# Performance work log

Measured on AMD Instinct MI355X. Metric: run time of the kernel, lower is better.

Reference implementation:

```python
import jax, jax.numpy as jnp
import numpy as np

G = 128          # number of point-cloud groups
DOWNSAMPLE = 256 # points per group
D = 256          # feature dim


def _pairwise_dist(x, y):
    # x: [G, n, d], y: [G, m, d] -> Euclidean distances [G, n, m]
    x2 = jnp.sum(x * x, axis=-1)[:, :, None]
    y2 = jnp.sum(y * y, axis=-1)[:, None, :]
    d2 = jnp.maximum(x2 + y2 - 2.0 * jnp.einsum('gnd,gmd->gnm', x, y), 0.0)
    # safe sqrt (zero diagonal has zero distance, avoid NaN grads)
    return jnp.where(d2 > 0, jnp.sqrt(jnp.where(d2 > 0, d2, 1.0)), 0.0)


def setup_inputs() -> dict:
    key = jax.random.key(0)
    k1, k2 = jax.random.split(key)
    inp = jax.random.normal(k1, (G * DOWNSAMPLE, D), dtype=jnp.float32)
    tgt = jax.random.normal(k2, (G * DOWNSAMPLE, D), dtype=jnp.float32)
    return {"input": inp, "target": tgt, "downsample": DOWNSAMPLE}


def reference(input, target, downsample):
    # MMDLoss.forward: reshape to (-1, downsample, D), batched energy distance, mean
    x = input.reshape(-1, downsample, input.shape[-1])   # [G, n, D]
    y = target.reshape(-1, downsample, target.shape[-1]) # [G, m, D]
    # Energy distance (geomloss 'energy' kernel k(x,y) = -||x-y||, uniform weights):
    # L = mean_ij ||x_i - y_j|| - 0.5 mean_ij ||x_i - x_j|| - 0.5 mean_ij ||y_i - y_j||
    d_xy = jnp.mean(_pairwise_dist(x, y), axis=(1, 2))  # [G]
    d_xx = jnp.mean(_pairwise_dist(x, x), axis=(1, 2))  # [G]
    d_yy = jnp.mean(_pairwise_dist(y, y), axis=(1, 2))  # [G]
    loss_per_group = d_xy - 0.5 * d_xx - 0.5 * d_yy
    return jnp.mean(loss_per_group)
```

## Files before the change

### kernel.cpp

```cpp
#include <hip/hip_runtime.h>
#include <hip/hip_bf16.h>
#include <stdint.h>
#include <string.h>

typedef __attribute__((ext_vector_type(8))) short short8;
typedef __attribute__((ext_vector_type(4))) float floatx4;

#define NPTS 256
#define DIM  256
#define TILE 128
#define BK   32
#define NIT  (DIM / BK)
#define LDSS 40

static __device__ __forceinline__ uint32_t cvtsq2(float a, float b, float& s) {
    __hip_bfloat162 h = __float22bfloat162_rn(float2{a, b});
    uint32_t d;
    memcpy(&d, &h, 4);
    const float lo = __builtin_bit_cast(float, d << 16);
    const float hi = __builtin_bit_cast(float, d & 0xFFFF0000u);
    s += lo * lo + hi * hi;
    return d;
}
static __device__ __forceinline__ uint4 cvt8(const float4 u, const float4 v, float& s) {
    uint4 r;
    r.x = cvtsq2(u.x, u.y, s); r.y = cvtsq2(u.z, u.w, s);
    r.z = cvtsq2(v.x, v.y, s); r.w = cvtsq2(v.z, v.w, s);
    return r;
}

__global__ __launch_bounds__(512, 4)
void mmd_pipe(const float* __restrict__ X, const float* __restrict__ Y,
              float* __restrict__ out, float scale, int G) {
    int g, t;
    const int f = blockIdx.x;
    if ((G & 7) == 0) { const int xcd = f & 7, j = f >> 3; g = (j / 10) * 8 + xcd; t = j % 10; }
    else              { g = f / 10; t = f % 10; }

    int ptype, ti, tj; float w;
    if (t < 4)      { ptype = 0; ti = t >> 1; tj = t & 1; w = 1.0f; }
    else if (t < 7) { int u = t - 4; ptype = 1; ti = (u == 2); tj = (u >= 1); w = (u == 1) ? -1.0f : -0.5f; }
    else            { int u = t - 7; ptype = 2; ti = (u == 2); tj = (u >= 1); w = (u == 1) ? -1.0f : -0.5f; }

    const float *Pf, *Qf;
    if (ptype == 0)      { Pf = X; Qf = Y; }
    else if (ptype == 1) { Pf = X; Qf = X; }
    else                 { Pf = Y; Qf = Y; }
    const bool symdiag = (ptype != 0) && (ti == tj);

    const size_t prow0 = (size_t)g * NPTS + (size_t)ti * TILE;
    const size_t qrow0 = (size_t)g * NPTS + (size_t)tj * TILE;

    __shared__ __align__(16) uint16_t As[2][TILE * LDSS];
    __shared__ __align__(16) uint16_t Bs[2][TILE * LDSS];
    __shared__ float rnorm[TILE];
    __shared__ float cnorm[TILE];
    __shared__ float wpart[8];

    const int tid  = threadIdx.x;
    const int lane = tid & 63;
    const int wv   = tid >> 6;
    const int quad = lane >> 4;
    const int l15  = lane & 15;
    const int rowbase = (wv & 3) * 32;
    const int colbase = (wv >> 2) * 64;

    const int prow = tid >> 2;
    const int pcol = (tid & 3) * 8;
    const float* gA = Pf + (prow0 + prow) * DIM + pcol;
    const float* gB = Qf + (qrow0 + prow) * DIM + pcol;
    const int woff = prow * LDSS + pcol;

    floatx4 acc[2][4];
    #pragma unroll
    for (int i = 0; i < 2; ++i)
        #pragma unroll
        for (int j = 0; j < 4; ++j) acc[i][j] = (floatx4)0.0f;

    float sqp = 0.0f, sqq = 0.0f;

    float4 ra0 = *(const float4*)(gA);
    float4 ra1 = *(const float4*)(gA + 4);
    float4 rb0 = *(const float4*)(gB);
    float4 rb1 = *(const float4*)(gB + 4);
    {
        const uint4 pa = cvt8(ra0, ra1, sqp);
        const uint4 pb = cvt8(rb0, rb1, sqq);
        *(uint4*)&As[0][woff] = pa;
        *(uint4*)&Bs[0][woff] = pb;
    }
    ra0 = *(const float4*)(gA + BK);
    ra1 = *(const float4*)(gA + BK + 4);
    rb0 = *(const float4*)(gB + BK);
    rb1 = *(const float4*)(gB + BK + 4);

    #pragma unroll
    for (int it = 0; it < NIT; ++it) {
        const int b = it & 1;
        __syncthreads();

        if (it < NIT - 1) {
            const uint4 pa = cvt8(ra0, ra1, sqp);
            const uint4 pb = cvt8(rb0, rb1, sqq);
            *(uint4*)&As[b ^ 1][woff] = pa;
            *(uint4*)&Bs[b ^ 1][woff] = pb;
        }
        if (it < NIT - 2) {
            const int k0 = (it + 2) * BK;
            ra0 = *(const float4*)(gA + k0);
            ra1 = *(const float4*)(gA + k0 + 4);
            rb0 = *(const float4*)(gB + k0);
            rb1 = *(const float4*)(gB + k0 + 4);
        }

        short8 af[2], bfr[4];
        #pragma unroll
        for (int mi = 0; mi < 2; ++mi)
            af[mi] = *(const short8*)&As[b][(rowbase + mi * 16 + l15) * LDSS + quad * 8];
        #pragma unroll
        for (int ni = 0; ni < 4; ++ni)
            bfr[ni] = *(const short8*)&Bs[b][(colbase + ni * 16 + l15) * LDSS + quad * 8];
        #pragma unroll
        for (int mi = 0; mi < 2; ++mi)
            #pragma unroll
            for (int ni = 0; ni < 4; ++ni)
                acc[mi][ni] = __builtin_amdgcn_mfma_f32_16x16x32_bf16(
                    af[mi], bfr[ni], acc[mi][ni], 0, 0, 0);
    }

    sqp += __shfl_xor(sqp, 1); sqp += __shfl_xor(sqp, 2);
    sqq += __shfl_xor(sqq, 1); sqq += __shfl_xor(sqq, 2);
    if ((tid & 3) == 0) { rnorm[prow] = sqp; cnorm[prow] = sqq; }
    __syncthreads();

    float lsum = 0.0f;
    #pragma unroll
    for (int mi = 0; mi < 2; ++mi) {
        #pragma unroll
        for (int i = 0; i < 4; ++i) {
            const int r = rowbase + mi * 16 + quad * 4 + i;
            const float rv = rnorm[r];
            #pragma unroll
            for (int ni = 0; ni < 4; ++ni) {
                const int c = colbase + ni * 16 + l15;
                float d2 = rv + cnorm[c] - 2.0f * acc[mi][ni][i];
                float s = sqrtf(fmaxf(d2, 0.0f));
                if (symdiag && (r == c)) s = 0.0f;
                lsum += s;
            }
        }
    }
    #pragma unroll
    for (int off = 32; off; off >>= 1) lsum += __shfl_down(lsum, off);
    if (lane == 0) wpart[wv] = lsum;
    __syncthreads();
    if (tid == 0) {
        float bs = 0.0f;
        #pragma unroll
        for (int i = 0; i < 8; ++i) bs += wpart[i];
        atomicAdd(out, bs * (w * scale));
    }
}

extern "C" void kernel_launch(void* const* d_in, const int* in_sizes, int n_in,
                              void* d_out, int out_size, void* d_ws, size_t ws_size,
                              hipStream_t stream) {
    const float* X = (const float*)d_in[0];
    const float* Y = (const float*)d_in[1];
    const int total_elems = in_sizes[0];
    const int G = total_elems / (NPTS * DIM);

    float* out = (float*)d_out;
    hipMemsetAsync(out, 0, sizeof(float) * out_size, stream);

    const float scale = 1.0f / ((float)NPTS * (float)NPTS * (float)G);
    mmd_pipe<<<10 * G, 512, 0, stream>>>(X, Y, out, scale, G);
}
```

Before: 122.0 us.

## Pre-convert inputs to bf16 with norms, then run LDS-DMA MFMA main kernel

Adds a prep kernel that converts X and Y to bf16 once in workspace and precomputes row norms. The main kernel then streams bf16 tiles into swizzled LDS using global_load_lds, with BK=64, 256 threads and a 4x4 MFMA tile per wave, and loads only one tile for symmetric diagonal blocks. This removes the repeated fp32 reads and conversions done in every tile block. The cost is an extra launch and a workspace round trip. The old fused path is kept as a fallback when no workspace is available.

```diff
diff --git a/kernel.cpp b/kernel.cpp
--- a/kernel.cpp
+++ b/kernel.cpp
@@ -5,13 +5,13 @@
 
 typedef __attribute__((ext_vector_type(8))) short short8;
 typedef __attribute__((ext_vector_type(4))) float floatx4;
+typedef unsigned short u16;
 
 #define NPTS 256
 #define DIM  256
 #define TILE 128
-#define BK   32
-#define NIT  (DIM / BK)
-#define LDSS 40
+#define BKN  64
+#define NITN (DIM / BKN)
 
 static __device__ __forceinline__ uint32_t cvtsq2(float a, float b, float& s) {
     __hip_bfloat162 h = __float22bfloat162_rn(float2{a, b});
@@ -25,9 +25,165 @@
 static __device__ __forceinline__ uint4 cvt8(const float4 u, const float4 v, float& s) {
     uint4 r;
     r.x = cvtsq2(u.x, u.y, s); r.y = cvtsq2(u.z, u.w, s);
-    r.z = cvtsq2(v.x, v.y, s); r.w = cvtsq2(v.z, v.w, s);
+    r.z = cvtsq2(v.x, v.w == v.w ? v.w : v.w, s), r.z = cvtsq2(v.x, v.y, s); r.w = cvtsq2(v.z, v.w, s);
     return r;
 }
+
+__global__ __launch_bounds__(256)
+void mmd_prep(const float* __restrict__ X, const float* __restrict__ Y,
+              u16* __restrict__ Zb, float* __restrict__ nrm,
+              int totalRows, int halfRows) {
+    const int gid = blockIdx.x * 256 + threadIdx.x;
+    const int row = gid >> 5;
+    if (row >= totalRows) return;
+    const int sub = gid & 31;
+    const float* src = (row < halfRows ? X + (size_t)row * DIM
+                                       : Y + (size_t)(row - halfRows) * DIM) + sub * 8;
+    const float4 a = *(const float4*)src;
+    const float4 b = *(const float4*)(src + 4);
+    float s = 0.0f;
+    uint4 p;
+    p.x = cvtsq2(a.x, a.y, s); p.y = cvtsq2(a.z, a.w, s);
+    p.z = cvtsq2(b.x, b.y, s); p.w = cvtsq2(b.z, b.w, s);
+    *(uint4*)(Zb + (size_t)row * DIM + sub * 8) = p;
+    s += __shfl_xor(s, 1); s += __shfl_xor(s, 2); s += __shfl_xor(s, 4);
+    s += __shfl_xor(s, 8); s += __shfl_xor(s, 16);
+    if (sub == 0) nrm[row] = s;
+}
+
+static __device__ __forceinline__ void stage_tile(
+    const u16* __restrict__ Zrow0,
+    u16* ldsbase,
+    int k0, int wv, int lane) {
+    #pragma unroll
+    for (int j = 0; j < 4; ++j) {
+        const int cid = (wv * 4 + j) * 64 + lane;
+        const int row = cid >> 3;
+        const int cs  = cid & 7;
+        const int cg  = cs ^ (row & 7);
+        const u16* src = Zrow0 + (size_t)row * DIM + k0 + cg * 8;
+        u16* dst = ldsbase + (size_t)(wv * 4 + j) * 512;
+        __builtin_amdgcn_global_load_lds(
+            (const __attribute__((address_space(1))) uint32_t*)src,
+            (__attribute__((address_space(3))) uint32_t*)dst, 16, 0, 0);
+    }
+}
+
+__global__ __launch_bounds__(256, 2)
+void mmd_main(const u16* __restrict__ Zb, const float* __restrict__ nrm,
+              float* __restrict__ out, float scale, int G) {
+    int g, t;
+    const int f = blockIdx.x;
+    if ((G & 7) == 0) { const int xcd = f & 7, j = f >> 3; g = (j / 10) * 8 + xcd; t = j % 10; }
+    else              { g = f / 10; t = f % 10; }
+
+    int ptype, ti, tj; float w;
+    if (t < 4)      { ptype = 0; ti = t >> 1; tj = t & 1; w = 1.0f; }
+    else if (t < 7) { int u = t - 4; ptype = 1; ti = (u == 2); tj = (u >= 1); w = (u == 1) ? -1.0f : -0.5f; }
+    else            { int u = t - 7; ptype = 2; ti = (u == 2); tj = (u >= 1); w = (u == 1) ? -1.0f : -0.5f; }
+
+    const int half = G * NPTS;
+    const int pbase = (ptype == 2) ? half : 0;
+    const int qbase = (ptype == 1) ? 0 : half;
+    const size_t prow0 = (size_t)pbase + (size_t)g * NPTS + (size_t)ti * TILE;
+    const size_t qrow0 = (size_t)qbase + (size_t)g * NPTS + (size_t)tj * TILE;
+    const bool symdiag = (ptype != 0) && (ti == tj);
+
+    const u16* ZP = Zb + prow0 * DIM;
+    const u16* ZQ = Zb + qrow0 * DIM;
+
+    __shared__ __align__(16) u16 As[2][TILE * BKN];
+    __shared__ __align__(16) u16 Bs[2][TILE * BKN];
+    __shared__ float rnormS[TILE];
+    __shared__ float cnormS[TILE];
+    __shared__ float wpart[4];
+
+    const int tid  = threadIdx.x;
+    const int lane = tid & 63;
+    const int wv   = tid >> 6;
+    const int quad = lane >> 4;
+    const int l15  = lane & 15;
+    const int wr   = (wv >> 1) * 64;
+    const int wc   = (wv & 1) * 64;
+    const int sw0  = (quad ^ (l15 & 7)) * 8;
+
+    floatx4 acc[4][4];
+    #pragma unroll
+    for (int i = 0; i < 4; ++i)
+        #pragma unroll
+        for (int j = 0; j < 4; ++j) acc[i][j] = (floatx4)0.0f;
+
+    if (tid < TILE) rnormS[tid] = nrm[prow0 + tid];
+    else            cnormS[tid - TILE] = nrm[qrow0 + (tid - TILE)];
+
+    stage_tile(ZP, As[0], 0, wv, lane);
+    if (!symdiag) stage_tile(ZQ, Bs[0], 0, wv, lane);
+
+    #pragma unroll
+    for (int it = 0; it < NITN; ++it) {
+        const int b = it & 1;
+        __syncthreads();
+
+        if (it + 1 < NITN) {
+            stage_tile(ZP, As[b ^ 1], (it + 1) * BKN, wv, lane);
+            if (!symdiag) stage_tile(ZQ, Bs[b ^ 1], (it + 1) * BKN, wv, lane);
+        }
+
+        const u16* abase = As[b];
+        const u16* bbase = symdiag ? As[b] : Bs[b];
+        #pragma unroll
+        for (int ks = 0; ks < 2; ++ks) {
+            const int kswz = ks * 32;
+            short8 af[4], bfv[4];
+            #pragma unroll
+            for (int mi = 0; mi < 4; ++mi) {
+                const int row = wr + mi * 16 + l15;
+                af[mi] = *(const short8*)&abase[row * BKN + (sw0 ^ kswz)];
+            }
+            #pragma unroll
+            for (int ni = 0; ni < 4; ++ni) {
+                const int row = wc + ni * 16 + l15;
+                bfv[ni] = *(const short8*)&bbase[row * BKN + (sw0 ^ kswz)];
+            }
+            #pragma unroll
+            for (int mi = 0; mi < 4; ++mi)
+                #pragma unroll
+                for (int ni = 0; ni < 4; ++ni)
+                    acc[mi][ni] = __builtin_amdgcn_mfma_f32_16x16x32_bf16(
+                        af[mi], bfv[ni], acc[mi][ni], 0, 0, 0);
+        }
+    }
+
+    float lsum = 0.0f;
+    #pragma unroll
+    for (int mi = 0; mi < 4; ++mi) {
+        #pragma unroll
+        for (int i = 0; i < 4; ++i) {
+            const int r = wr + mi * 16 + quad * 4 + i;
+            const float rv = rnormS[r];
+            #pragma unroll
+            for (int ni = 0; ni < 4; ++ni) {
+                const int c = wc + ni * 16 + l15;
+                float d2 = rv + cnormS[c] - 2.0f * acc[mi][ni][i];
+                float s = sqrtf(fmaxf(d2, 0.0f));
+                if (symdiag && (r == c)) s = 0.0f;
+                lsum += s;
+            }
+        }
+    }
+    #pragma unroll
+    for (int off = 32; off; off >>= 1) lsum += __shfl_down(lsum, off);
+    if (lane == 0) wpart[wv] = lsum;
+    __syncthreads();
+    if (tid == 0) {
+        float bs = wpart[0] + wpart[1] + wpart[2] + wpart[3];
+        atomicAdd(out, bs * (w * scale));
+    }
+}
+
+#define BK   32
+#define NIT  (DIM / BK)
+#define LDSS 40
 
 __global__ __launch_bounds__(512, 4)
 void mmd_pipe(const float* __restrict__ X, const float* __restrict__ Y,
@@ -84,8 +240,11 @@
     float4 rb0 = *(const float4*)(gB);
     float4 rb1 = *(const float4*)(gB + 4);
     {
-        const uint4 pa = cvt8(ra0, ra1, sqp);
-        const uint4 pb = cvt8(rb0, rb1, sqq);
+        uint4 pa, pb;
+        pa.x = cvtsq2(ra0.x, ra0.y, sqp); pa.y = cvtsq2(ra0.z, ra0.w, sqp);
+        pa.z = cvtsq2(ra1.x, ra1.y, sqp); pa.w = cvtsq2(ra1.z, ra1.w, sqp);
+        pb.x = cvtsq2(rb0.x, rb0.y, sqq); pb.y = cvtsq2(rb0.z, rb0.w, sqq);
+        pb.z = cvtsq2(rb1.x, rb1.y, sqq); pb.w = cvtsq2(rb1.z, rb1.w, sqq);
         *(uint4*)&As[0][woff] = pa;
         *(uint4*)&Bs[0][woff] = pb;
     }
@@ -100,8 +259,11 @@
         __syncthreads();
 
         if (it < NIT - 1) {
-            const uint4 pa = cvt8(ra0, ra1, sqp);
-            const uint4 pb = cvt8(rb0, rb1, sqq);
+            uint4 pa, pb;
+            pa.x = cvtsq2(ra0.x, ra0.y, sqp); pa.y = cvtsq2(ra0.z, ra0.w, sqp);
+            pa.z = cvtsq2(ra1.x, ra1.y, sqp); pa.w = cvtsq2(ra1.z, ra1.w, sqp);
+            pb.x = cvtsq2(rb0.x, rb0.y, sqq); pb.y = cvtsq2(rb0.z, rb0.w, sqq);
+            pb.z = cvtsq2(rb1.x, rb1.y, sqq); pb.w = cvtsq2(rb1.z, rb1.w, sqq);
             *(uint4*)&As[b ^ 1][woff] = pa;
             *(uint4*)&Bs[b ^ 1][woff] = pb;
         }
@@ -174,5 +336,18 @@
     hipMemsetAsync(out, 0, sizeof(float) * out_size, stream);
 
     const float scale = 1.0f / ((float)NPTS * (float)NPTS * (float)G);
-    mmd_pipe<<<10 * G, 512, 0, stream>>>(X, Y, out, scale, G);
-}
+
+    const size_t rows = (size_t)2 * G * NPTS;
+    const size_t zb_bytes  = rows * DIM * sizeof(u16);
+    const size_t nrm_bytes = rows * sizeof(float);
+
+    if (d_ws != nullptr && ws_size >= zb_bytes + nrm_bytes) {
+        u16* Zb = (u16*)d_ws;
+        float* nrm = (float*)((char*)d_ws + zb_bytes);
+        const int pblocks = (int)(rows / 8);
+        mmd_prep<<<pblocks, 256, 0, stream>>>(X, Y, Zb, nrm, (int)rows, G * NPTS);
+        mmd_main<<<10 * G, 256, 0, stream>>>(Zb, nrm, out, scale, G);
+    } else {
+        mmd_pipe<<<10 * G, 512, 0, stream>>>(X, Y, out, scale, G);
+    }
+}
```

Result: slower. 133.2 us (+9.2%).

## Compute each full 256x256 pair matrix per block with swizzled LDS

Applied to the files above, without the earlier changes.

Adds a kernel in which each block computes one whole 256x256 distance matrix (XY, XX or YY) for a group, giving 3 blocks per group instead of 10 blocks of 128x128 tiles. The symmetric cases load and convert only one operand and reuse it for both sides, and LDS uses an XOR swizzle instead of padding. The aim is to remove redundant global loads and bf16 conversions. In exchange it uses 128 accumulator registers per thread, runs at lower occupancy (launch bounds 2) and launches far fewer blocks, so load balance and latency hiding may suffer. The old kernel stays as a fallback when G is not a multiple of 8.

```diff
diff --git a/kernel.cpp b/kernel.cpp
--- a/kernel.cpp
+++ b/kernel.cpp
@@ -5,13 +5,12 @@
 
 typedef __attribute__((ext_vector_type(8))) short short8;
 typedef __attribute__((ext_vector_type(4))) float floatx4;
+typedef unsigned short u16;
 
 #define NPTS 256
 #define DIM  256
-#define TILE 128
-#define BK   32
-#define NIT  (DIM / BK)
-#define LDSS 40
+#define BKF  32
+#define NSL  (DIM / BKF)
 
 static __device__ __forceinline__ uint32_t cvtsq2(float a, float b, float& s) {
     __hip_bfloat162 h = __float22bfloat162_rn(float2{a, b});
@@ -22,12 +21,170 @@
     s += lo * lo + hi * hi;
     return d;
 }
-static __device__ __forceinline__ uint4 cvt8(const float4 u, const float4 v, float& s) {
-    uint4 r;
-    r.x = cvtsq2(u.x, u.y, s); r.y = cvtsq2(u.z, u.w, s);
-    r.z = cvtsq2(v.x, v.y, s); r.w = cvtsq2(v.z, v.w, s);
-    return r;
+
+__global__ __launch_bounds__(512, 2)
+void mmd_fused(const float* __restrict__ X, const float* __restrict__ Y,
+               float* __restrict__ out, float scale, int G) {
+    int g, t;
+    const int f = blockIdx.x;
+    { const int xcd = f & 7, j = f >> 3; g = (j / 3) * 8 + xcd; t = j % 3; }
+    const float w  = (t == 0) ? 1.0f : -0.5f;
+    const bool sym = (t != 0);
+    const float* Pf = (t == 2) ? Y : X;
+    const float* Qf = (t == 1) ? X : Y;
+    const size_t base = (size_t)g * NPTS * DIM;
+
+    __shared__ __align__(16) u16 As[2][NPTS * BKF];
+    __shared__ __align__(16) u16 Bs[2][NPTS * BKF];
+    __shared__ float rnormS[NPTS];
+    __shared__ float cnormS[NPTS];
+    __shared__ float wpart[8];
+
+    const int tid  = threadIdx.x;
+    const int lane = tid & 63;
+    const int wv   = tid >> 6;
+    const int quad = lane >> 4;
+    const int l15  = lane & 15;
+    const int wr   = (wv & 3) * 64;
+    const int wc   = (wv >> 2) * 128;
+    const int rsw  = (quad ^ ((l15 >> 1) & 3)) * 8;
+
+    const int srow = tid >> 1;
+    const int scol = (tid & 1) * 16;
+    const float* gP = Pf + base + (size_t)srow * DIM + scol;
+    const float* gQ = Qf + base + (size_t)srow * DIM + scol;
+    const int c0   = (tid & 1) * 2;
+    const int sswz = (srow >> 1) & 3;
+    const int wo0  = srow * BKF + ((c0    ) ^ sswz) * 8;
+    const int wo1  = srow * BKF + ((c0 + 1) ^ sswz) * 8;
+
+    floatx4 acc[4][8];
+    #pragma unroll
+    for (int i = 0; i < 4; ++i)
+        #pragma unroll
+        for (int j = 0; j < 8; ++j) acc[i][j] = (floatx4)0.0f;
+
+    float sqp = 0.0f, sqq = 0.0f;
+    float4 ra[4], rb[4];
+
+    #pragma unroll
+    for (int q = 0; q < 4; ++q) ra[q] = *(const float4*)(gP + q * 4);
+    if (!sym) {
+        #pragma unroll
+        for (int q = 0; q < 4; ++q) rb[q] = *(const float4*)(gQ + q * 4);
+    }
+    {
+        uint4 u0, u1;
+        u0.x = cvtsq2(ra[0].x, ra[0].y, sqp); u0.y = cvtsq2(ra[0].z, ra[0].w, sqp);
+        u0.z = cvtsq2(ra[1].x, ra[1].y, sqp); u0.w = cvtsq2(ra[1].z, ra[1].w, sqp);
+        u1.x = cvtsq2(ra[2].x, ra[2].y, sqp); u1.y = cvtsq2(ra[2].z, ra[2].w, sqp);
+        u1.z = cvtsq2(ra[3].x, ra[3].y, sqp); u1.w = cvtsq2(ra[3].z, ra[3].w, sqp);
+        *(uint4*)&As[0][wo0] = u0; *(uint4*)&As[0][wo1] = u1;
+        if (!sym) {
+            uint4 v0, v1;
+            v0.x = cvtsq2(rb[0].x, rb[0].y, sqq); v0.y = cvtsq2(rb[0].z, rb[0].w, sqq);
+            v0.z = cvtsq2(rb[1].x, rb[1].y, sqq); v0.w = cvtsq2(rb[1].z, rb[1].w, sqq);
+            v1.x = cvtsq2(rb[2].x, rb[2].y, sqq); v1.y = cvtsq2(rb[2].z, rb[2].w, sqq);
+            v1.z = cvtsq2(rb[3].x, rb[3].y, sqq); v1.w = cvtsq2(rb[3].z, rb[3].w, sqq);
+            *(uint4*)&Bs[0][wo0] = v0; *(uint4*)&Bs[0][wo1] = v1;
+        }
+    }
+    #pragma unroll
+    for (int q = 0; q < 4; ++q) ra[q] = *(const float4*)(gP + BKF + q * 4);
+    if (!sym) {
+        #pragma unroll
+        for (int q = 0; q < 4; ++q) rb[q] = *(const float4*)(gQ + BKF + q * 4);
+    }
+
+    #pragma unroll
+    for (int it = 0; it < NSL; ++it) {
+        const int b = it & 1;
+        __syncthreads();
+
+        if (it < NSL - 1) {
+            uint4 u0, u1;
+            u0.x = cvtsq2(ra[0].x, ra[0].y, sqp); u0.y = cvtsq2(ra[0].z, ra[0].w, sqp);
+            u0.z = cvtsq2(ra[1].x, ra[1].y, sqp); u0.w = cvtsq2(ra[1].z, ra[1].w, sqp);
+            u1.x = cvtsq2(ra[2].x, ra[2].y, sqp); u1.y = cvtsq2(ra[2].z, ra[2].w, sqp);
+            u1.z = cvtsq2(ra[3].x, ra[3].y, sqp); u1.w = cvtsq2(ra[3].z, ra[3].w, sqp);
+            *(uint4*)&As[b ^ 1][wo0] = u0; *(uint4*)&As[b ^ 1][wo1] = u1;
+            if (!sym) {
+                uint4 v0, v1;
+                v0.x = cvtsq2(rb[0].x, rb[0].y, sqq); v0.y = cvtsq2(rb[0].z, rb[0].w, sqq);
+                v0.z = cvtsq2(rb[1].x, rb[1].y, sqq); v0.w = cvtsq2(rb[1].z, rb[1].w, sqq);
+                v1.x = cvtsq2(rb[2].x, rb[2].y, sqq); v1.y = cvtsq2(rb[2].z, rb[2].w, sqq);
+                v1.z = cvtsq2(rb[3].x, rb[3].y, sqq); v1.w = cvtsq2(rb[3].z, rb[3].w, sqq);
+                *(uint4*)&Bs[b ^ 1][wo0] = v0; *(uint4*)&Bs[b ^ 1][wo1] = v1;
+            }
+        }
+        if (it < NSL - 2) {
+            const int k0 = (it + 2) * BKF;
+            #pragma unroll
+            for (int q = 0; q < 4; ++q) ra[q] = *(const float4*)(gP + k0 + q * 4);
+            if (!sym) {
+                #pragma unroll
+                for (int q = 0; q < 4; ++q) rb[q] = *(const float4*)(gQ + k0 + q * 4);
+            }
+        }
+
+        const u16* ab = As[b];
+        const u16* bb = sym ? As[b] : Bs[b];
+        short8 af[4], bfv[8];
+        #pragma unroll
+        for (int mi = 0; mi < 4; ++mi)
+            af[mi] = *(const short8*)&ab[(wr + mi * 16 + l15) * BKF + rsw];
+        #pragma unroll
+        for (int ni = 0; ni < 8; ++ni)
+            bfv[ni] = *(const short8*)&bb[(wc + ni * 16 + l15) * BKF + rsw];
+        #pragma unroll
+        for (int mi = 0; mi < 4; ++mi)
+            #pragma unroll
+            for (int ni = 0; ni < 8; ++ni)
+                acc[mi][ni] = __builtin_amdgcn_mfma_f32_16x16x32_bf16(
+                    af[mi], bfv[ni], acc[mi][ni], 0, 0, 0);
+    }
+
+    sqp += __shfl_xor(sqp, 1);
+    sqq += __shfl_xor(sqq, 1);
+    if ((tid & 1) == 0) {
+        rnormS[srow] = sqp;
+        cnormS[srow] = sym ? sqp : sqq;
+    }
+    __syncthreads();
+
+    float lsum = 0.0f;
+    #pragma unroll
+    for (int mi = 0; mi < 4; ++mi) {
+        #pragma unroll
+        for (int i = 0; i < 4; ++i) {
+            const int r = wr + mi * 16 + quad * 4 + i;
+            const float rv = rnormS[r];
+            #pragma unroll
+            for (int ni = 0; ni < 8; ++ni) {
+                const int c = wc + ni * 16 + l15;
+                float d2 = rv + cnormS[c] - 2.0f * acc[mi][ni][i];
+                float s = sqrtf(fmaxf(d2, 0.0f));
+                if (sym && (r == c)) s = 0.0f;
+                lsum += s;
+            }
+        }
+    }
+    #pragma unroll
+    for (int off = 32; off; off >>= 1) lsum += __shfl_down(lsum, off);
+    if (lane == 0) wpart[wv] = lsum;
+    __syncthreads();
+    if (tid == 0) {
+        float bs = 0.0f;
+        #pragma unroll
+        for (int i = 0; i < 8; ++i) bs += wpart[i];
+        atomicAdd(out, bs * (w * scale));
+    }
 }
+
+#define TILE 128
+#define BK   32
+#define NIT  (DIM / BK)
+#define LDSS 40
 
 __global__ __launch_bounds__(512, 4)
 void mmd_pipe(const float* __restrict__ X, const float* __restrict__ Y,
@@ -84,8 +241,11 @@
     float4 rb0 = *(const float4*)(gB);
     float4 rb1 = *(const float4*)(gB + 4);
     {
-        const uint4 pa = cvt8(ra0, ra1, sqp);
-        const uint4 pb = cvt8(rb0, rb1, sqq);
+        uint4 pa, pb;
+        pa.x = cvtsq2(ra0.x, ra0.y, sqp); pa.y = cvtsq2(ra0.z, ra0.w, sqp);
+        pa.z = cvtsq2(ra1.x, ra1.y, sqp); pa.w = cvtsq2(ra1.z, ra1.w, sqp);
+        pb.x = cvtsq2(rb0.x, rb0.y, sqq); pb.y = cvtsq2(rb0.z, rb0.w, sqq);
+        pb.z = cvtsq2(rb1.x, rb1.y, sqq); pb.w = cvtsq2(rb1.z, rb1.w, sqq);
         *(uint4*)&As[0][woff] = pa;
         *(uint4*)&Bs[0][woff] = pb;
     }
@@ -100,8 +260,11 @@
         __syncthreads();
 
         if (it < NIT - 1) {
-            const uint4 pa = cvt8(ra0, ra1, sqp);
-            const uint4 pb = cvt8(rb0, rb1, sqq);
+            uint4 pa, pb;
+            pa.x = cvtsq2(ra0.x, ra0.y, sqp); pa.y = cvtsq2(ra0.z, ra0.w, sqp);
+            pa.z = cvtsq2(ra1.x, ra1.y, sqp); pa.w = cvtsq2(ra1.z, ra1.w, sqp);
+            pb.x = cvtsq2(rb0.x, rb0.y, sqq); pb.y = cvtsq2(rb0.z, rb0.w, sqq);
+            pb.z = cvtsq2(rb1.x, rb1.y, sqq); pb.w = cvtsq2(rb1.z, rb1.w, sqq);
             *(uint4*)&As[b ^ 1][woff] = pa;
             *(uint4*)&Bs[b ^ 1][woff] = pb;
         }
@@ -174,5 +337,10 @@
     hipMemsetAsync(out, 0, sizeof(float) * out_size, stream);
 
     const float scale = 1.0f / ((float)NPTS * (float)NPTS * (float)G);
-    mmd_pipe<<<10 * G, 512, 0, stream>>>(X, Y, out, scale, G);
+
+    if ((G & 7) == 0) {
+        mmd_fused<<<3 * G, 512, 0, stream>>>(X, Y, out, scale, G);
+    } else {
+        mmd_pipe<<<10 * G, 512, 0, stream>>>(X, Y, out, scale, G);
+    }
 }
```

Result: slower. 196.7 us (+61.2%).

## XOR-swizzle LDS tiles and skip duplicate B loads on symmetric diagonal tiles

Applied to the files above, without the earlier changes.

Replaces the padded LDS row stride (40) with an unpadded 32-element stride plus an XOR swizzle of 8-element chunks, to avoid bank conflicts while shrinking shared memory. On symmetric diagonal tiles (xx/yy with ti==tj), the B operand is now read from the A buffer, so the second global load, bf16 conversion and LDS store are skipped and column norms reuse the row norms. The extra branches are uniform per block, so they should add little divergence.

```diff
diff --git a/kernel.cpp b/kernel.cpp
--- a/kernel.cpp
+++ b/kernel.cpp
@@ -11,7 +11,6 @@
 #define TILE 128
 #define BK   32
 #define NIT  (DIM / BK)
-#define LDSS 40
 
 static __device__ __forceinline__ uint32_t cvtsq2(float a, float b, float& s) {
     __hip_bfloat162 h = __float22bfloat162_rn(float2{a, b});
@@ -21,12 +20,6 @@
     const float hi = __builtin_bit_cast(float, d & 0xFFFF0000u);
     s += lo * lo + hi * hi;
     return d;
-}
-static __device__ __forceinline__ uint4 cvt8(const float4 u, const float4 v, float& s) {
-    uint4 r;
-    r.x = cvtsq2(u.x, u.y, s); r.y = cvtsq2(u.z, u.w, s);
-    r.z = cvtsq2(v.x, v.y, s); r.w = cvtsq2(v.z, v.w, s);
-    return r;
 }
 
 __global__ __launch_bounds__(512, 4)
@@ -51,8 +44,8 @@
     const size_t prow0 = (size_t)g * NPTS + (size_t)ti * TILE;
     const size_t qrow0 = (size_t)g * NPTS + (size_t)tj * TILE;
 
-    __shared__ __align__(16) uint16_t As[2][TILE * LDSS];
-    __shared__ __align__(16) uint16_t Bs[2][TILE * LDSS];
+    __shared__ __align__(16) uint16_t As[2][TILE * BK];
+    __shared__ __align__(16) uint16_t Bs[2][TILE * BK];
     __shared__ float rnorm[TILE];
     __shared__ float cnorm[TILE];
     __shared__ float wpart[8];
@@ -64,12 +57,13 @@
     const int l15  = lane & 15;
     const int rowbase = (wv & 3) * 32;
     const int colbase = (wv >> 2) * 64;
+    const int rsw = (quad ^ ((l15 >> 1) & 3)) * 8;
 
     const int prow = tid >> 2;
-    const int pcol = (tid & 3) * 8;
-    const float* gA = Pf + (prow0 + prow) * DIM + pcol;
-    const float* gB = Qf + (qrow0 + prow) * DIM + pcol;
-    const int woff = prow * LDSS + pcol;
+    const int pchk = tid & 3;
+    const float* gA = Pf + (prow0 + prow) * DIM + pchk * 8;
+    const float* gB = Qf + (qrow0 + prow) * DIM + pchk * 8;
+    const int woff = prow * BK + ((pchk ^ ((prow >> 1) & 3)) * 8);
 
     floatx4 acc[2][4];
     #pragma unroll
@@ -81,18 +75,26 @@
 
     float4 ra0 = *(const float4*)(gA);
     float4 ra1 = *(const float4*)(gA + 4);
-    float4 rb0 = *(const float4*)(gB);
-    float4 rb1 = *(const float4*)(gB + 4);
+    float4 rb0, rb1;
+    if (!symdiag) { rb0 = *(const float4*)(gB); rb1 = *(const float4*)(gB + 4); }
     {
-        const uint4 pa = cvt8(ra0, ra1, sqp);
-        const uint4 pb = cvt8(rb0, rb1, sqq);
+        uint4 pa;
+        pa.x = cvtsq2(ra0.x, ra0.y, sqp); pa.y = cvtsq2(ra0.z, ra0.w, sqp);
+        pa.z = cvtsq2(ra1.x, ra1.y, sqp); pa.w = cvtsq2(ra1.z, ra1.w, sqp);
         *(uint4*)&As[0][woff] = pa;
-        *(uint4*)&Bs[0][woff] = pb;
+        if (!symdiag) {
+            uint4 pb;
+            pb.x = cvtsq2(rb0.x, rb0.y, sqq); pb.y = cvtsq2(rb0.z, rb0.w, sqq);
+            pb.z = cvtsq2(rb1.x, rb1.y, sqq); pb.w = cvtsq2(rb1.z, rb1.w, sqq);
+            *(uint4*)&Bs[0][woff] = pb;
+        }
     }
     ra0 = *(const float4*)(gA + BK);
     ra1 = *(const float4*)(gA + BK + 4);
-    rb0 = *(const float4*)(gB + BK);
-    rb1 = *(const float4*)(gB + BK + 4);
+    if (!symdiag) {
+        rb0 = *(const float4*)(gB + BK);
+        rb1 = *(const float4*)(gB + BK + 4);
+    }
 
     #pragma unroll
     for (int it = 0; it < NIT; ++it) {
@@ -100,26 +102,36 @@
         __syncthreads();
 
         if (it < NIT - 1) {
-            const uint4 pa = cvt8(ra0, ra1, sqp);
-            const uint4 pb = cvt8(rb0, rb1, sqq);
+            uint4 pa;
+            pa.x = cvtsq2(ra0.x, ra0.y, sqp); pa.y = cvtsq2(ra0.z, ra0.w, sqp);
+            pa.z = cvtsq2(ra1.x, ra1.y, sqp); pa.w = cvtsq2(ra1.z, ra1.w, sqp);
             *(uint4*)&As[b ^ 1][woff] = pa;
-            *(uint4*)&Bs[b ^ 1][woff] = pb;
+            if (!symdiag) {
+                uint4 pb;
+                pb.x = cvtsq2(rb0.x, rb0.y, sqq); pb.y = cvtsq2(rb0.z, rb0.w, sqq);
+                pb.z = cvtsq2(rb1.x, rb1.y, sqq); pb.w = cvtsq2(rb1.z, rb1.w, sqq);
+                *(uint4*)&Bs[b ^ 1][woff] = pb;
+            }
         }
         if (it < NIT - 2) {
             const int k0 = (it + 2) * BK;
             ra0 = *(const float4*)(gA + k0);
             ra1 = *(const float4*)(gA + k0 + 4);
-            rb0 = *(const float4*)(gB + k0);
-            rb1 = *(const float4*)(gB + k0 + 4);
+            if (!symdiag) {
+                rb0 = *(const float4*)(gB + k0);
+                rb1 = *(const float4*)(gB + k0 + 4);
+            }
         }
 
+        const uint16_t* ab = As[b];
+        const uint16_t* bb = symdiag ? As[b] : Bs[b];
         short8 af[2], bfr[4];
         #pragma unroll
         for (int mi = 0; mi < 2; ++mi)
-            af[mi] = *(const short8*)&As[b][(rowbase + mi * 16 + l15) * LDSS + quad * 8];
+            af[mi] = *(const short8*)&ab[(rowbase + mi * 16 + l15) * BK + rsw];
         #pragma unroll
         for (int ni = 0; ni < 4; ++ni)
-            bfr[ni] = *(const short8*)&Bs[b][(colbase + ni * 16 + l15) * LDSS + quad * 8];
+            bfr[ni] = *(const short8*)&bb[(colbase + ni * 16 + l15) * BK + rsw];
         #pragma unroll
         for (int mi = 0; mi < 2; ++mi)
             #pragma unroll
@@ -129,8 +141,11 @@
     }
 
     sqp += __shfl_xor(sqp, 1); sqp += __shfl_xor(sqp, 2);
-    sqq += __shfl_xor(sqq, 1); sqq += __shfl_xor(sqq, 2);
-    if ((tid & 3) == 0) { rnorm[prow] = sqp; cnorm[prow] = sqq; }
+    if (!symdiag) { sqq += __shfl_xor(sqq, 1); sqq += __shfl_xor(sqq, 2); }
+    if ((tid & 3) == 0) {
+        rnorm[prow] = sqp;
+        cnorm[prow] = symdiag ? sqp : sqq;
+    }
     __syncthreads();
 
     float lsum = 0.0f;
```

New measurement: 181.5 us. +48.8%, slower.
